# Optimization experiments

Hardware: AMD Instinct MI355X
Metric: run time of the kernel (lower is better)

Reference implementation:

```python
import jax, jax.numpy as jnp
import numpy as np

B, Q_LEN, K_LEN = 2, 2048, 2048
Q_CH, K_CH = 1024, 1024
H, D = 16, 64  # head_num, head_dim = q_channels // head_num
TEMPERATURE = (H * D) ** 0.5  # use_tube=False -> sqrt(1024)=32


def setup_inputs() -> dict:
    key = jax.random.key(0)
    ks = jax.random.split(key, 14)
    s = 0.02
    return {
        "q": jax.random.normal(ks[0], (B, Q_LEN, Q_CH), jnp.float32),
        "k": jax.random.normal(ks[1], (B, K_LEN, K_CH), jnp.float32),
        "v": jax.random.normal(ks[2], (B, K_LEN, K_CH), jnp.float32),
        "mask": jax.random.randint(ks[3], (B, Q_LEN, K_LEN), 0, 2) == 1,
        "attn_bias": jax.random.normal(ks[4], (B, H, Q_LEN, K_LEN), jnp.float32),
        # weights stored [in, out] (math-equivalent to torch Linear's x @ W.T + b)
        "Wq": jax.random.normal(ks[5], (Q_CH, H * D), jnp.float32) * s,
        "bq": jnp.zeros((H * D,), jnp.float32),
        "Wk": jax.random.normal(ks[6], (K_CH, H * D), jnp.float32) * s,
        "bk": jnp.zeros((H * D,), jnp.float32),
        "Wv": jax.random.normal(ks[7], (K_CH, H * D), jnp.float32) * s,
        "bv": jnp.zeros((H * D,), jnp.float32),
        "Wo": jax.random.normal(ks[8], (H * D, Q_CH), jnp.float32) * s,
        "bo": jnp.zeros((Q_CH,), jnp.float32),
    }


def reference(q, k, v, mask, attn_bias, Wq, bq, Wk, bk, Wv, bv, Wo, bo):
    b, q_len = q.shape[0], q.shape[1]
    k_len = k.shape[1]
    # projections + head split: [b, len, H, D] -> [b, H, len, D]
    qh = (q @ Wq + bq).reshape(b, q_len, H, D).transpose(0, 2, 1, 3)
    kh = (k @ Wk + bk).reshape(b, k_len, H, D).transpose(0, 2, 1, 3)
    vh = (v @ Wv + bv).reshape(b, k_len, H, D).transpose(0, 2, 1, 3)
    # scores [b, H, q_len, k_len]
    scores = jnp.einsum("bhqd,bhkd->bhqk", qh, kh) / TEMPERATURE + attn_bias
    scores = jnp.where(mask[:, None, :, :], -jnp.inf, scores)
    attn = jax.nn.softmax(scores, axis=-1)
    # dropout is identity in eval / deterministic reference
    out = jnp.einsum("bhqk,bhkd->bhqd", attn, vh)
    out = out.transpose(0, 2, 1, 3).reshape(b, q_len, H * D)
    out = out @ Wo + bo
    return out, attn
```

## Files before the change

kernel.cpp:

```cpp
#include <hip/hip_runtime.h>
#include <hip/hip_bf16.h>


typedef __attribute__((ext_vector_type(8))) short bf16x8;
typedef __attribute__((ext_vector_type(8))) _Float16 f16x8;
typedef __attribute__((ext_vector_type(4))) float f32x4;
typedef __attribute__((ext_vector_type(4))) int i32x4;
typedef __attribute__((ext_vector_type(4))) _Float16 f16x4;
typedef unsigned short u16;

#define NB 2
#define QL 2048
#define KL 2048
#define CH 1024
#define NH 16
#define HD 64
#define SH_STRIDE 2600

__device__ __forceinline__ u16 f2bf(float f){
  unsigned u = __float_as_uint(f);
  u += 0x7fffu + ((u >> 16) & 1u);
  return (u16)(u >> 16);
}
__device__ __forceinline__ u16 f2h(float f){
  _Float16 h = (_Float16)f;
  return *(u16*)&h;
}

__global__ void k_detect(const unsigned int* __restrict__ m, int* __restrict__ flag){
  unsigned v = m[threadIdx.x];
  unsigned long long b = __ballot(v > 1u);
  __shared__ int r[4];
  if ((threadIdx.x & 63) == 0) r[threadIdx.x >> 6] = (b != 0ULL);
  __syncthreads();
  if (threadIdx.x == 0) *flag = (r[0] | r[1] | r[2] | r[3]);
}

__global__ __launch_bounds__(256) void k_maskpack(const void* __restrict__ maskp, const int* __restrict__ flag,
                                                  unsigned* __restrict__ mbits){
  const int idx = blockIdx.x*256 + threadIdx.x;
  unsigned out = 0;
  if (*flag){
    const unsigned* m8 = (const unsigned*)maskp + (size_t)idx*8;
    #pragma unroll
    for (int j=0;j<8;++j){
      unsigned wv = m8[j];
      out |= ((wv & 1u) | ((wv>>7)&2u) | ((wv>>14)&4u) | ((wv>>21)&8u)) << (4*j);
    }
  } else {
    const i32x4* m32 = (const i32x4*)maskp + (size_t)idx*8;
    #pragma unroll
    for (int j=0;j<8;++j){
      i32x4 v = m32[j];
      out |= (unsigned)((v[0]&1) | ((v[1]&1)<<1) | ((v[2]&1)<<2) | ((v[3]&1)<<3)) << (4*j);
    }
  }
  mbits[idx] = out;
}

__global__ __launch_bounds__(256) void k_transpose(const float* __restrict__ Wq, const float* __restrict__ Wk,
                                                   const float* __restrict__ Wv, const float* __restrict__ Wo,
                                                   u16* __restrict__ wt){
  const float* src = blockIdx.z==0 ? Wq : blockIdx.z==1 ? Wk : blockIdx.z==2 ? Wv : Wo;
  u16* dst = wt + (size_t)blockIdx.z * CH * CH;
  __shared__ float t[32][33];
  const int x = blockIdx.x*32, y = blockIdx.y*32;
  const int tx = threadIdx.x & 31, ty = threadIdx.x >> 5;
  #pragma unroll
  for (int j=0;j<32;j+=8) t[ty+j][tx] = src[(size_t)(y+ty+j)*CH + x + tx];
  __syncthreads();
  #pragma unroll
  for (int j=0;j<32;j+=8) dst[(size_t)(x+ty+j)*CH + y + tx] = f2bf(t[tx][ty+j]);
}

__global__ __launch_bounds__(256) void k_gemm_qkv(const float* __restrict__ q, const float* __restrict__ k,
                                                  const float* __restrict__ v, const u16* __restrict__ wt,
                                                  const float* __restrict__ bq, const float* __restrict__ bk,
                                                  const float* __restrict__ bv,
                                                  u16* __restrict__ qh, u16* __restrict__ kh, u16* __restrict__ vt){
  const int z = blockIdx.z;
  const float* A = z==0 ? q : z==1 ? k : v;
  const u16* Bt = wt + (size_t)z*CH*CH;
  const float* bias = z==0 ? bq : z==1 ? bk : bv;
  u16* Cp = z==0 ? qh : z==1 ? kh : vt;
  const float scale = (z==0) ? 0.03125f : 1.0f;

  __shared__ u16 As[64][72];
  __shared__ u16 Bs[64][72];
  const int m0 = blockIdx.y*64, n0 = blockIdx.x*64;
  const int tid = threadIdx.x, lane = tid & 63, w = tid >> 6;
  const int wm = w >> 1, wn = w & 1;
  const int lr = lane & 15, lg = lane >> 4;
  f32x4 acc[2][2] = {};
  for (int k0 = 0; k0 < CH; k0 += 64){
    #pragma unroll
    for (int j=0;j<4;++j){
      int idx = tid + 256*j, r = idx >> 4, c = (idx & 15)*4;
      float4 vv = *(const float4*)&A[(size_t)(m0+r)*CH + k0 + c];
      ushort4 s; s.x=f2bf(vv.x); s.y=f2bf(vv.y); s.z=f2bf(vv.z); s.w=f2bf(vv.w);
      *(ushort4*)&As[r][c] = s;
    }
    #pragma unroll
    for (int j=0;j<2;++j){
      int idx = tid + 256*j, r = idx >> 3, c = (idx & 7)*8;
      *(uint4*)&Bs[r][c] = *(const uint4*)&Bt[(size_t)(n0+r)*CH + k0 + c];
    }
    __syncthreads();
    #pragma unroll
    for (int kk=0; kk<2; ++kk){
      bf16x8 a0 = *(const bf16x8*)&As[wm*32      + lr][kk*32 + lg*8];
      bf16x8 a1 = *(const bf16x8*)&As[wm*32 + 16 + lr][kk*32 + lg*8];
      bf16x8 b0 = *(const bf16x8*)&Bs[wn*32      + lr][kk*32 + lg*8];
      bf16x8 b1 = *(const bf16x8*)&Bs[wn*32 + 16 + lr][kk*32 + lg*8];
      acc[0][0] = __builtin_amdgcn_mfma_f32_16x16x32_bf16(a0,b0,acc[0][0],0,0,0);
      acc[0][1] = __builtin_amdgcn_mfma_f32_16x16x32_bf16(a0,b1,acc[0][1],0,0,0);
      acc[1][0] = __builtin_amdgcn_mfma_f32_16x16x32_bf16(a1,b0,acc[1][0],0,0,0);
      acc[1][1] = __builtin_amdgcn_mfma_f32_16x16x32_bf16(a1,b1,acc[1][1],0,0,0);
    }
    __syncthreads();
  }
  #pragma unroll
  for (int fi=0;fi<2;++fi)
  #pragma unroll
  for (int fj=0;fj<2;++fj)
  #pragma unroll
  for (int r=0;r<4;++r){
    int row = m0 + wm*32 + fi*16 + lg*4 + r;
    int col = n0 + wn*32 + fj*16 + lr;
    float val = (acc[fi][fj][r] + bias[col]) * scale;
    int bb = row >> 11, ll = row & 2047, hh = col >> 6, dd = col & 63;
    if (z < 2){
      Cp[(((size_t)(bb*NH+hh)*QL + ll) << 6) + dd] = f2bf(val);
    } else {
      Cp[(((size_t)(bb*NH+hh) << 6) + dd)*KL + ll] = f2h(val);
    }
  }
}

__global__ __launch_bounds__(256) void k_gemm_out(const u16* __restrict__ Ap, const u16* __restrict__ Bt,
                                                  const float* __restrict__ bias, float* __restrict__ Cp){
  __shared__ u16 As[64][72];
  __shared__ u16 Bs[64][72];
  const int m0 = blockIdx.y*64, n0 = blockIdx.x*64;
  const int tid = threadIdx.x, lane = tid & 63, w = tid >> 6;
  const int wm = w >> 1, wn = w & 1;
  const int lr = lane & 15, lg = lane >> 4;
  f32x4 acc[2][2] = {};
  for (int k0 = 0; k0 < CH; k0 += 64){
    #pragma unroll
    for (int j=0;j<2;++j){
      int idx = tid + 256*j, r = idx >> 3, c = (idx & 7)*8;
      *(uint4*)&As[r][c] = *(const uint4*)&Ap[(size_t)(m0+r)*CH + k0 + c];
      *(uint4*)&Bs[r][c] = *(const uint4*)&Bt[(size_t)(n0+r)*CH + k0 + c];
    }
    __syncthreads();
    #pragma unroll
    for (int kk=0; kk<2; ++kk){
      bf16x8 a0 = *(const bf16x8*)&As[wm*32      + lr][kk*32 + lg*8];
      bf16x8 a1 = *(const bf16x8*)&As[wm*32 + 16 + lr][kk*32 + lg*8];
      bf16x8 b0 = *(const bf16x8*)&Bs[wn*32      + lr][kk*32 + lg*8];
      bf16x8 b1 = *(const bf16x8*)&Bs[wn*32 + 16 + lr][kk*32 + lg*8];
      acc[0][0] = __builtin_amdgcn_mfma_f32_16x16x32_bf16(a0,b0,acc[0][0],0,0,0);
      acc[0][1] = __builtin_amdgcn_mfma_f32_16x16x32_bf16(a0,b1,acc[0][1],0,0,0);
      acc[1][0] = __builtin_amdgcn_mfma_f32_16x16x32_bf16(a1,b0,acc[1][0],0,0,0);
      acc[1][1] = __builtin_amdgcn_mfma_f32_16x16x32_bf16(a1,b1,acc[1][1],0,0,0);
    }
    __syncthreads();
  }
  #pragma unroll
  for (int fi=0;fi<2;++fi)
  #pragma unroll
  for (int fj=0;fj<2;++fj)
  #pragma unroll
  for (int r=0;r<4;++r){
    int row = m0 + wm*32 + fi*16 + lg*4 + r;
    int col = n0 + wn*32 + fj*16 + lr;
    Cp[(size_t)row*CH + col] = acc[fi][fj][r] + bias[col];
  }
}

template<int BITS>
__global__ __launch_bounds__(1024, 1) void k_attn(const u16* __restrict__ qh, const u16* __restrict__ kh,
                                              const _Float16* __restrict__ vt, const float* __restrict__ bias,
                                              const void* __restrict__ maskp, const int* __restrict__ flag,
                                              const unsigned* __restrict__ mbits,
                                              float* __restrict__ attn, u16* __restrict__ ao){
  __shared__ _Float16 Sh[16][SH_STRIDE];
  __shared__ float osum[8][16][17];
  __shared__ float wsum[16][16];
  __shared__ float inv_l[16];
  const int qt = BITS ? blockIdx.x : blockIdx.y;
  const int h  = BITS ? blockIdx.y : blockIdx.x;
  const int b  = blockIdx.z;
  const int q0 = qt*16, bh = b*NH + h;
  const int tid = threadIdx.x, lane = tid & 63, w = tid >> 6;
  const int lr = lane & 15, lg = lane >> 4;
  const u16* qb = qh + ((size_t)bh*QL + q0)*HD;
  const bf16x8 qf0 = *(const bf16x8*)&qb[lr*HD +      lg*8];
  const bf16x8 qf1 = *(const bf16x8*)&qb[lr*HD + 32 + lg*8];
  const float* bb = bias + ((size_t)bh*QL + q0)*KL;
  const u16* khb = kh + (size_t)bh*KL*HD;
  const _Float16* vtb = vt + (size_t)bh*HD*KL;
  const int c0 = w*128;

  f32x4 bi[8];
  unsigned mwd[8];
  #pragma unroll
  for (int ct=0; ct<8; ++ct){
    const int cb = c0 + ct*16 + lg*4;
    bi[ct] = *(const f32x4*)&bb[(size_t)lr*KL + cb];
    if (BITS) mwd[ct] = mbits[((size_t)b*QL + q0 + lr)*(KL/32) + (cb>>5)];
  }
  const int isbool = BITS ? 0 : *flag;
  const unsigned char* mb8 = (const unsigned char*)maskp + ((size_t)b*QL + q0)*KL;
  const int* mb32 = (const int*)maskp + ((size_t)b*QL + q0)*KL;

  float ps = 0.f;
  #pragma unroll
  for (int ct=0; ct<8; ++ct){
    const int cb = c0 + ct*16 + lg*4;
    f32x4 acc = bi[ct];
    const int kcol = c0 + ct*16 + lr;
    bf16x8 kf0 = *(const bf16x8*)&khb[(size_t)kcol*HD +      lg*8];
    bf16x8 kf1 = *(const bf16x8*)&khb[(size_t)kcol*HD + 32 + lg*8];
    acc = __builtin_amdgcn_mfma_f32_16x16x32_bf16(kf0, qf0, acc, 0,0,0);
    acc = __builtin_amdgcn_mfma_f32_16x16x32_bf16(kf1, qf1, acc, 0,0,0);
    unsigned msel;
    i32x4 mv;
    if (BITS){
      msel = (mwd[ct] >> (cb & 31)) & 0xFu;
    } else if (isbool){
      unsigned mw = *(const unsigned*)&mb8[(size_t)lr*KL + cb];
      msel = (mw&1u) | ((mw>>7)&2u) | ((mw>>14)&4u) | ((mw>>21)&8u);
    } else {
      mv = *(const i32x4*)&mb32[(size_t)lr*KL + cb];
      msel = (unsigned)((mv[0]&1) | ((mv[1]&1)<<1) | ((mv[2]&1)<<2) | ((mv[3]&1)<<3));
    }
    f16x4 sv;
    #pragma unroll
    for (int r=0;r<4;++r){
      float e = ((msel >> r) & 1u) ? 0.f : __expf(acc[r]);
      sv[r] = (_Float16)e;
      ps += e;
    }
    *(f16x4*)&Sh[lr][cb] = sv;
  }
  ps += __shfl_xor(ps, 16);
  ps += __shfl_xor(ps, 32);
  if (lane < 16) wsum[w][lr] = ps;
  __syncthreads();
  if (tid < 16){
    float s = 0.f;
    #pragma unroll
    for (int ww=0; ww<16; ++ww) s += wsum[ww][tid];
    inv_l[tid] = 1.f / s;
  }
  __syncthreads();

  if (w < 8){
    const int d0 = (w & 3)*16, kb0 = (w >> 2)*1024;
    f32x4 oacc = {};
    #pragma unroll
    for (int kb=0; kb<4; ++kb){
      f16x8 vf[8];
      #pragma unroll
      for (int i=0;i<8;++i)
        vf[i] = *(const f16x8*)&vtb[(size_t)(d0+lr)*KL + kb0 + kb*256 + i*32 + lg*8];
      #pragma unroll
      for (int i=0;i<8;++i){
        f16x8 a = *(const f16x8*)&Sh[lr][kb0 + kb*256 + i*32 + lg*8];
        oacc = __builtin_amdgcn_mfma_f32_16x16x32_f16(a, vf[i], oacc, 0,0,0);
      }
    }
    #pragma unroll
    for (int r=0;r<4;++r) osum[w][lg*4+r][lr] = oacc[r];
  } else {
    float* ob = attn + ((size_t)bh*QL + q0)*KL;
    const int r0 = (w - 8)*2;
    #pragma unroll
    for (int rr=0; rr<2; ++rr){
      const int row = r0 + rr;
      const float ivr = inv_l[row];
      #pragma unroll
      for (int ch=0; ch<8; ++ch){
        f16x4 hv = *(const f16x4*)&Sh[row][ch*256 + lane*4];
        f32x4 v;
        v[0]=(float)hv[0]*ivr; v[1]=(float)hv[1]*ivr; v[2]=(float)hv[2]*ivr; v[3]=(float)hv[3]*ivr;
        *(f32x4*)&ob[(size_t)row*KL + ch*256 + lane*4] = v;
      }
    }
  }
  __syncthreads();

  {
    const int row = tid >> 6, d = tid & 63;
    float o = (osum[d >> 4][row][d & 15] + osum[4 + (d >> 4)][row][d & 15]) * inv_l[row];
    ao[((size_t)b*QL + q0 + row)*CH + h*HD + d] = f2bf(o);
  }
}

extern "C" void kernel_launch(void* const* d_in, const int* in_sizes, int n_in,
                              void* d_out, int out_size, void* d_ws, size_t ws_size,
                              hipStream_t stream){
  const float* q    = (const float*)d_in[0];
  const float* k    = (const float*)d_in[1];
  const float* v    = (const float*)d_in[2];
  const void*  mask = d_in[3];
  const float* bias = (const float*)d_in[4];
  const float* Wq   = (const float*)d_in[5];
  const float* bq   = (const float*)d_in[6];
  const float* Wk   = (const float*)d_in[7];
  const float* bk   = (const float*)d_in[8];
  const float* Wv   = (const float*)d_in[9];
  const float* bv   = (const float*)d_in[10];
  const float* Wo   = (const float*)d_in[11];
  const float* bo   = (const float*)d_in[12];

  char* wsb = (char*)d_ws;
  int* flag = (int*)wsb;
  u16* qh = (u16*)(wsb + 256);
  u16* kh = (u16*)(wsb + 256 + 1*8388608);
  u16* vt = (u16*)(wsb + 256 + 2*8388608);
  u16* ao = (u16*)(wsb + 256 + 3*8388608);
  u16* wt = (u16*)(wsb + 256 + 4*8388608);
  unsigned* mbits = (unsigned*)(wsb + 256 + 5*8388608);
  const size_t need_bits = 256 + 5ull*8388608 + 1048576;
  const bool usebits = (ws_size >= need_bits);

  float* out  = (float*)d_out;
  float* attn = out + (size_t)NB*QL*CH;

  k_detect<<<1, 256, 0, stream>>>((const unsigned int*)mask, flag);
  if (usebits)
    k_maskpack<<<dim3(1024), 256, 0, stream>>>(mask, flag, mbits);
  k_transpose<<<dim3(32,32,4), 256, 0, stream>>>(Wq, Wk, Wv, Wo, wt);
  k_gemm_qkv<<<dim3(16,64,3), 256, 0, stream>>>(q, k, v, wt, bq, bk, bv, qh, kh, vt);
  if (usebits)
    k_attn<1><<<dim3(128,16,2), 1024, 0, stream>>>(qh, kh, (const _Float16*)vt, bias, mask, flag, mbits, attn, ao);
  else
    k_attn<0><<<dim3(16,128,2), 1024, 0, stream>>>(qh, kh, (const _Float16*)vt, bias, mask, flag, mbits, attn, ao);
  k_gemm_out<<<dim3(16,64), 256, 0, stream>>>(ao, wt + 3145728, bo, out);
}
```

Before: 602.2 us.

## Split fused attention into QK-softmax and PV kernels via fp16 probability buffer

Replaces the single fused attention kernel with two kernels. The first computes scores, masked exp and normalization and writes normalized fp16 probabilities to a large workspace buffer. The second reads them back, runs the PV matmul and expands them to the fp32 attn output. The intent is presumably to shrink per-kernel LDS and register pressure and improve scheduling, at the cost of an extra 256MB round trip through global memory. The padded shared array in the PV kernel appears to force one block per CU. The split path is taken only if the workspace is large enough.

```diff
diff --git a/kernel.cpp b/kernel.cpp
--- a/kernel.cpp
+++ b/kernel.cpp
@@ -176,6 +176,132 @@
     int row = m0 + wm*32 + fi*16 + lg*4 + r;
     int col = n0 + wn*32 + fj*16 + lr;
     Cp[(size_t)row*CH + col] = acc[fi][fj][r] + bias[col];
+  }
+}
+
+__global__ __launch_bounds__(1024, 1) void k_qk(const u16* __restrict__ qh, const u16* __restrict__ kh,
+                                                const float* __restrict__ bias,
+                                                const unsigned* __restrict__ mbits,
+                                                _Float16* __restrict__ S16){
+  __shared__ _Float16 Sh[16][SH_STRIDE];
+  __shared__ float wsum[16][16];
+  __shared__ float inv_l[16];
+  const int qt = blockIdx.x, h = blockIdx.y, b = blockIdx.z;
+  const int q0 = qt*16, bh = b*NH + h;
+  const int tid = threadIdx.x, lane = tid & 63, w = tid >> 6;
+  const int lr = lane & 15, lg = lane >> 4;
+  const u16* qb = qh + ((size_t)bh*QL + q0)*HD;
+  const bf16x8 qf0 = *(const bf16x8*)&qb[lr*HD +      lg*8];
+  const bf16x8 qf1 = *(const bf16x8*)&qb[lr*HD + 32 + lg*8];
+  const float* bb = bias + ((size_t)bh*QL + q0)*KL;
+  const u16* khb = kh + (size_t)bh*KL*HD;
+  const int c0 = w*128;
+
+  f32x4 bi[8];
+  unsigned mwd[8];
+  #pragma unroll
+  for (int ct=0; ct<8; ++ct){
+    const int cb = c0 + ct*16 + lg*4;
+    bi[ct] = *(const f32x4*)&bb[(size_t)lr*KL + cb];
+    mwd[ct] = mbits[((size_t)b*QL + q0 + lr)*(KL/32) + (cb>>5)];
+  }
+
+  float ps = 0.f;
+  #pragma unroll
+  for (int ct=0; ct<8; ++ct){
+    const int cb = c0 + ct*16 + lg*4;
+    f32x4 acc = bi[ct];
+    const int kcol = c0 + ct*16 + lr;
+    bf16x8 kf0 = *(const bf16x8*)&khb[(size_t)kcol*HD +      lg*8];
+    bf16x8 kf1 = *(const bf16x8*)&khb[(size_t)kcol*HD + 32 + lg*8];
+    acc = __builtin_amdgcn_mfma_f32_16x16x32_bf16(kf0, qf0, acc, 0,0,0);
+    acc = __builtin_amdgcn_mfma_f32_16x16x32_bf16(kf1, qf1, acc, 0,0,0);
+    const unsigned msel = (mwd[ct] >> (cb & 31)) & 0xFu;
+    f16x4 sv;
+    #pragma unroll
+    for (int r=0;r<4;++r){
+      float e = ((msel >> r) & 1u) ? 0.f : __expf(acc[r]);
+      sv[r] = (_Float16)e;
+      ps += e;
+    }
+    *(f16x4*)&Sh[lr][cb] = sv;
+  }
+  ps += __shfl_xor(ps, 16);
+  ps += __shfl_xor(ps, 32);
+  if (lane < 16) wsum[w][lr] = ps;
+  __syncthreads();
+  if (tid < 16){
+    float s = 0.f;
+    #pragma unroll
+    for (int ww=0; ww<16; ++ww) s += wsum[ww][tid];
+    inv_l[tid] = 1.f / s;
+  }
+  __syncthreads();
+
+  _Float16* sg = S16 + ((size_t)bh*QL + q0 + w)*KL;
+  const float ivw = inv_l[w];
+  #pragma unroll
+  for (int ch=0; ch<4; ++ch){
+    f16x8 hv = *(const f16x8*)&Sh[w][ch*512 + lane*8];
+    f16x8 ov;
+    #pragma unroll
+    for (int j=0;j<8;++j) ov[j] = (_Float16)((float)hv[j] * ivw);
+    *(f16x8*)&sg[ch*512 + lane*8] = ov;
+  }
+}
+
+__global__ __launch_bounds__(1024, 1) void k_pv(const _Float16* __restrict__ S16, const _Float16* __restrict__ vt,
+                                                float* __restrict__ attn, u16* __restrict__ ao){
+  __shared__ float osum[8][16][17];
+  __shared__ float pad[18500];
+  const int qt = blockIdx.x, h = blockIdx.y, b = blockIdx.z;
+  const int q0 = qt*16, bh = b*NH + h;
+  const int tid = threadIdx.x, lane = tid & 63, w = tid >> 6;
+  const int lr = lane & 15, lg = lane >> 4;
+  ((volatile float*)pad)[tid] = 0.f;
+  const _Float16* sb = S16 + ((size_t)bh*QL + q0)*KL;
+
+  if (w < 8){
+    const int d0 = (w & 3)*16, kb0 = (w >> 2)*1024;
+    const _Float16* vtb = vt + (size_t)bh*HD*KL;
+    f32x4 oacc = {};
+    #pragma unroll
+    for (int kb=0; kb<4; ++kb){
+      f16x8 vf[8], af[8];
+      #pragma unroll
+      for (int i=0;i<8;++i){
+        vf[i] = *(const f16x8*)&vtb[(size_t)(d0+lr)*KL + kb0 + kb*256 + i*32 + lg*8];
+        af[i] = *(const f16x8*)&sb[(size_t)lr*KL + kb0 + kb*256 + i*32 + lg*8];
+      }
+      #pragma unroll
+      for (int i=0;i<8;++i)
+        oacc = __builtin_amdgcn_mfma_f32_16x16x32_f16(af[i], vf[i], oacc, 0,0,0);
+    }
+    #pragma unroll
+    for (int r=0;r<4;++r) osum[w][lg*4+r][lr] = oacc[r];
+  } else {
+    float* ob = attn + ((size_t)bh*QL + q0)*KL;
+    const int r0 = (w - 8)*2;
+    #pragma unroll
+    for (int rr=0; rr<2; ++rr){
+      const int row = r0 + rr;
+      const _Float16* sr = sb + (size_t)row*KL;
+      float* orow = ob + (size_t)row*KL;
+      #pragma unroll
+      for (int ch=0; ch<8; ++ch){
+        f16x4 hv = *(const f16x4*)&sr[ch*256 + lane*4];
+        f32x4 v;
+        v[0]=(float)hv[0]; v[1]=(float)hv[1]; v[2]=(float)hv[2]; v[3]=(float)hv[3];
+        *(f32x4*)&orow[ch*256 + lane*4] = v;
+      }
+    }
+  }
+  __syncthreads();
+
+  {
+    const int row = tid >> 6, d = tid & 63;
+    float o = osum[d >> 4][row][d & 15] + osum[4 + (d >> 4)][row][d & 15];
+    ao[((size_t)b*QL + q0 + row)*CH + h*HD + d] = f2bf(o);
   }
 }
 
@@ -291,7 +417,6 @@
     }
   }
   __syncthreads();
-
   {
     const int row = tid >> 6, d = tid & 63;
     float o = (osum[d >> 4][row][d & 15] + osum[4 + (d >> 4)][row][d & 15]) * inv_l[row];
@@ -324,8 +449,11 @@
   u16* ao = (u16*)(wsb + 256 + 3*8388608);
   u16* wt = (u16*)(wsb + 256 + 4*8388608);
   unsigned* mbits = (unsigned*)(wsb + 256 + 5*8388608);
-  const size_t need_bits = 256 + 5ull*8388608 + 1048576;
-  const bool usebits = (ws_size >= need_bits);
+  _Float16* S16 = (_Float16*)(wsb + 256 + 5*8388608 + 1048576);
+  const size_t need_bits  = 256 + 5ull*8388608 + 1048576;
+  const size_t need_split = need_bits + (size_t)NB*NH*QL*KL*2;
+  const bool usebits  = (ws_size >= need_bits);
+  const bool usesplit = (ws_size >= need_split);
 
   float* out  = (float*)d_out;
   float* attn = out + (size_t)NB*QL*CH;
@@ -335,9 +463,13 @@
     k_maskpack<<<dim3(1024), 256, 0, stream>>>(mask, flag, mbits);
   k_transpose<<<dim3(32,32,4), 256, 0, stream>>>(Wq, Wk, Wv, Wo, wt);
   k_gemm_qkv<<<dim3(16,64,3), 256, 0, stream>>>(q, k, v, wt, bq, bk, bv, qh, kh, vt);
-  if (usebits)
+  if (usesplit){
+    k_qk<<<dim3(128,16,2), 1024, 0, stream>>>(qh, kh, bias, mbits, S16);
+    k_pv<<<dim3(128,16,2), 1024, 0, stream>>>(S16, (const _Float16*)vt, attn, ao);
+  } else if (usebits){
     k_attn<1><<<dim3(128,16,2), 1024, 0, stream>>>(qh, kh, (const _Float16*)vt, bias, mask, flag, mbits, attn, ao);
-  else
+  } else {
     k_attn<0><<<dim3(16,128,2), 1024, 0, stream>>>(qh, kh, (const _Float16*)vt, bias, mask, flag, mbits, attn, ao);
+  }
   k_gemm_out<<<dim3(16,64), 256, 0, stream>>>(ao, wt + 3145728, bo, out);
 }
```

Measured after the change: 766.0 us. 1.27x slower.

## Pre-convert QKV inputs to bf16 and use XOR-swizzled LDS GEMM

Applied to the files above, without the earlier changes.

Adds a separate kernel that converts q, k, v from fp32 to bf16 once. The QKV projection GEMM then loads bf16 tiles directly instead of converting fp32 inside every tile load, which the old code repeated for each of the 16 column blocks. A shared GEMM body uses an XOR-swizzled 64x64 LDS layout instead of padded rows and serves both the QKV and output projections. The trade-off is an extra kernel launch, about 25 MB of added workspace traffic, and a dependency on workspace size.

```diff
diff --git a/kernel.cpp b/kernel.cpp
--- a/kernel.cpp
+++ b/kernel.cpp
@@ -56,6 +56,21 @@
     }
   }
   mbits[idx] = out;
+}
+
+__global__ __launch_bounds__(256) void k_cvt(const float* __restrict__ q, const float* __restrict__ k,
+                                             const float* __restrict__ v,
+                                             u16* __restrict__ qc, u16* __restrict__ kc, u16* __restrict__ vc){
+  const float* in = blockIdx.y==0 ? q : blockIdx.y==1 ? k : v;
+  u16* out = blockIdx.y==0 ? qc : blockIdx.y==1 ? kc : vc;
+  const size_t i = ((size_t)blockIdx.x*256 + threadIdx.x)*8;
+  float4 lo = *(const float4*)&in[i];
+  float4 hi = *(const float4*)&in[i+4];
+  ushort4 a, b;
+  a.x=f2bf(lo.x); a.y=f2bf(lo.y); a.z=f2bf(lo.z); a.w=f2bf(lo.w);
+  b.x=f2bf(hi.x); b.y=f2bf(hi.y); b.z=f2bf(hi.z); b.w=f2bf(hi.w);
+  *(ushort4*)&out[i] = a;
+  *(ushort4*)&out[i+4] = b;
 }
 
 __global__ __launch_bounds__(256) void k_transpose(const float* __restrict__ Wq, const float* __restrict__ Wk,
@@ -71,6 +86,77 @@
   __syncthreads();
   #pragma unroll
   for (int j=0;j<32;j+=8) dst[(size_t)(x+ty+j)*CH + y + tx] = f2bf(t[tx][ty+j]);
+}
+
+__device__ __forceinline__ void gemm64_body(const u16* __restrict__ A, const u16* __restrict__ Bt,
+                                            const float* __restrict__ bias, void* __restrict__ Cp,
+                                            int clay, float scale, int m0, int n0){
+  __shared__ u16 As[64][64];
+  __shared__ u16 Bs[64][64];
+  const int tid = threadIdx.x, lane = tid & 63, w = tid >> 6;
+  const int wm = w >> 1, wn = w & 1;
+  const int lr = lane & 15, lg = lane >> 4;
+  f32x4 acc[2][2] = {};
+  for (int k0 = 0; k0 < CH; k0 += 64){
+    #pragma unroll
+    for (int i=0;i<2;++i){
+      const int r = i*32 + (tid>>3), c8 = tid & 7;
+      const int sw = (c8 ^ (r&7))*8;
+      *(uint4*)&As[r][sw] = *(const uint4*)&A[(size_t)(m0+r)*CH + k0 + c8*8];
+      *(uint4*)&Bs[r][sw] = *(const uint4*)&Bt[(size_t)(n0+r)*CH + k0 + c8*8];
+    }
+    __syncthreads();
+    #pragma unroll
+    for (int kk=0; kk<2; ++kk){
+      const int c8a = ((kk*4 + lg) ^ (lr&7))*8;
+      bf16x8 a0 = *(const bf16x8*)&As[wm*32      + lr][c8a];
+      bf16x8 a1 = *(const bf16x8*)&As[wm*32 + 16 + lr][c8a];
+      bf16x8 b0 = *(const bf16x8*)&Bs[wn*32      + lr][c8a];
+      bf16x8 b1 = *(const bf16x8*)&Bs[wn*32 + 16 + lr][c8a];
+      acc[0][0] = __builtin_amdgcn_mfma_f32_16x16x32_bf16(a0,b0,acc[0][0],0,0,0);
+      acc[0][1] = __builtin_amdgcn_mfma_f32_16x16x32_bf16(a0,b1,acc[0][1],0,0,0);
+      acc[1][0] = __builtin_amdgcn_mfma_f32_16x16x32_bf16(a1,b0,acc[1][0],0,0,0);
+      acc[1][1] = __builtin_amdgcn_mfma_f32_16x16x32_bf16(a1,b1,acc[1][1],0,0,0);
+    }
+    __syncthreads();
+  }
+  #pragma unroll
+  for (int fi=0;fi<2;++fi)
+  #pragma unroll
+  for (int fj=0;fj<2;++fj)
+  #pragma unroll
+  for (int r=0;r<4;++r){
+    int row = m0 + wm*32 + fi*16 + lg*4 + r;
+    int col = n0 + wn*32 + fj*16 + lr;
+    float val = (acc[fi][fj][r] + bias[col]) * scale;
+    if (clay == 2){
+      ((float*)Cp)[(size_t)row*CH + col] = val;
+    } else {
+      int bb = row >> 11, ll = row & 2047, hh = col >> 6, dd = col & 63;
+      if (clay == 0)
+        ((u16*)Cp)[(((size_t)(bb*NH+hh)*QL + ll) << 6) + dd] = f2bf(val);
+      else
+        ((u16*)Cp)[(((size_t)(bb*NH+hh) << 6) + dd)*KL + ll] = f2h(val);
+    }
+  }
+}
+
+__global__ __launch_bounds__(256) void k_gemm_qkv2(const u16* __restrict__ qc, const u16* __restrict__ kc,
+                                                   const u16* __restrict__ vc, const u16* __restrict__ wt,
+                                                   const float* __restrict__ bq, const float* __restrict__ bk,
+                                                   const float* __restrict__ bv,
+                                                   u16* __restrict__ qh, u16* __restrict__ kh, u16* __restrict__ vt){
+  const int z = blockIdx.z;
+  const u16* A = z==0 ? qc : z==1 ? kc : vc;
+  const u16* Bt = wt + (size_t)z*CH*CH;
+  const float* bias = z==0 ? bq : z==1 ? bk : bv;
+  void* Cp = z==0 ? (void*)qh : z==1 ? (void*)kh : (void*)vt;
+  gemm64_body(A, Bt, bias, Cp, z==2 ? 1 : 0, z==0 ? 0.03125f : 1.0f, blockIdx.y*64, blockIdx.x*64);
+}
+
+__global__ __launch_bounds__(256) void k_gemm_out2(const u16* __restrict__ ao, const u16* __restrict__ wto,
+                                                   const float* __restrict__ bo, float* __restrict__ out){
+  gemm64_body(ao, wto, bo, out, 2, 1.0f, blockIdx.y*64, blockIdx.x*64);
 }
 
 __global__ __launch_bounds__(256) void k_gemm_qkv(const float* __restrict__ q, const float* __restrict__ k,
@@ -84,7 +170,6 @@
   const float* bias = z==0 ? bq : z==1 ? bk : bv;
   u16* Cp = z==0 ? qh : z==1 ? kh : vt;
   const float scale = (z==0) ? 0.03125f : 1.0f;
-
   __shared__ u16 As[64][72];
   __shared__ u16 Bs[64][72];
   const int m0 = blockIdx.y*64, n0 = blockIdx.x*64;
@@ -129,11 +214,8 @@
     int col = n0 + wn*32 + fj*16 + lr;
     float val = (acc[fi][fj][r] + bias[col]) * scale;
     int bb = row >> 11, ll = row & 2047, hh = col >> 6, dd = col & 63;
-    if (z < 2){
-      Cp[(((size_t)(bb*NH+hh)*QL + ll) << 6) + dd] = f2bf(val);
-    } else {
-      Cp[(((size_t)(bb*NH+hh) << 6) + dd)*KL + ll] = f2h(val);
-    }
+    if (z < 2) Cp[(((size_t)(bb*NH+hh)*QL + ll) << 6) + dd] = f2bf(val);
+    else       Cp[(((size_t)(bb*NH+hh) << 6) + dd)*KL + ll] = f2h(val);
   }
 }
 
@@ -291,7 +373,6 @@
     }
   }
   __syncthreads();
-
   {
     const int row = tid >> 6, d = tid & 63;
     float o = (osum[d >> 4][row][d & 15] + osum[4 + (d >> 4)][row][d & 15]) * inv_l[row];
@@ -324,8 +405,13 @@
   u16* ao = (u16*)(wsb + 256 + 3*8388608);
   u16* wt = (u16*)(wsb + 256 + 4*8388608);
   unsigned* mbits = (unsigned*)(wsb + 256 + 5*8388608);
+  u16* qc = (u16*)(wsb + 256 + 5*8388608 + 1048576);
+  u16* kc = qc + (size_t)NB*QL*CH;
+  u16* vc = kc + (size_t)NB*QL*CH;
   const size_t need_bits = 256 + 5ull*8388608 + 1048576;
+  const size_t need_conv = need_bits + 3ull*NB*QL*CH*2;
   const bool usebits = (ws_size >= need_bits);
+  const bool useconv = (ws_size >= need_conv);
 
   float* out  = (float*)d_out;
   float* attn = out + (size_t)NB*QL*CH;
@@ -334,10 +420,18 @@
   if (usebits)
     k_maskpack<<<dim3(1024), 256, 0, stream>>>(mask, flag, mbits);
   k_transpose<<<dim3(32,32,4), 256, 0, stream>>>(Wq, Wk, Wv, Wo, wt);
-  k_gemm_qkv<<<dim3(16,64,3), 256, 0, stream>>>(q, k, v, wt, bq, bk, bv, qh, kh, vt);
+  if (useconv){
+    k_cvt<<<dim3(2048,3), 256, 0, stream>>>(q, k, v, qc, kc, vc);
+    k_gemm_qkv2<<<dim3(16,64,3), 256, 0, stream>>>(qc, kc, vc, wt, bq, bk, bv, qh, kh, vt);
+  } else {
+    k_gemm_qkv<<<dim3(16,64,3), 256, 0, stream>>>(q, k, v, wt, bq, bk, bv, qh, kh, vt);
+  }
   if (usebits)
     k_attn<1><<<dim3(128,16,2), 1024, 0, stream>>>(qh, kh, (const _Float16*)vt, bias, mask, flag, mbits, attn, ao);
   else
     k_attn<0><<<dim3(16,128,2), 1024, 0, stream>>>(qh, kh, (const _Float16*)vt, bias, mask, flag, mbits, attn, ao);
-  k_gemm_out<<<dim3(16,64), 256, 0, stream>>>(ao, wt + 3145728, bo, out);
-}
+  if (useconv)
+    k_gemm_out2<<<dim3(16,64), 256, 0, stream>>>(ao, wt + 3145728, bo, out);
+  else
+    k_gemm_out<<<dim3(16,64), 256, 0, stream>>>(ao, wt + 3145728, bo, out);
+}
```

New measurement: 567.8 us. 5.7% less time.
